# Kernel optimization log

Measured on AMD Instinct MI355X. Metric: run time of the kernel, lower is better.

Reference implementation:

```python
import jax, jax.numpy as jnp
import numpy as np

N_NODES = 100000
N_EDGES = 1600000
D_IN, D_HID, D_OUT = 128, 128, 64


def setup_inputs() -> dict:
    key = jax.random.key(0)
    k1, k2, k3, k4 = jax.random.split(key, 4)
    x = jax.random.normal(k1, (N_NODES, D_IN), dtype=jnp.float32)
    edge_index = jax.random.randint(k2, (2, N_EDGES), 0, N_NODES, dtype=jnp.int64)
    # Glorot-style weights, zero bias (GCNConv defaults: weight + bias)
    W1 = jax.random.normal(k3, (D_IN, D_HID), dtype=jnp.float32) * (1.0 / np.sqrt(D_IN))
    b1 = jnp.zeros((D_HID,), dtype=jnp.float32)
    W2 = jax.random.normal(k4, (D_HID, D_OUT), dtype=jnp.float32) * (1.0 / np.sqrt(D_HID))
    b2 = jnp.zeros((D_OUT,), dtype=jnp.float32)
    return {"x": x, "edge_index": edge_index, "W1": W1, "b1": b1, "W2": W2, "b2": b2}


def reference(x, edge_index, W1, b1, W2, b2):
    n = x.shape[0]
    src, dst = edge_index[0], edge_index[1]
    # GCN symmetric normalization, add_self_loops=False
    ones = jnp.ones((src.shape[0],), dtype=x.dtype)
    deg = jax.ops.segment_sum(ones, dst, num_segments=n)
    deg_inv_sqrt = jnp.where(deg > 0, jax.lax.rsqrt(jnp.maximum(deg, 1.0)), 0.0)
    norm = deg_inv_sqrt[src] * deg_inv_sqrt[dst]  # [E]

    def gcn_conv(h, W, b):
        h = h @ W                                   # [N, d_out] transform first
        msg = h[src] * norm[:, None]                # [E, d_out] gather + scale
        agg = jax.ops.segment_sum(msg, dst, num_segments=n)  # scatter-add
        return agg + b

    h = jax.nn.relu(gcn_conv(x, W1, b1))
    # dropout(p=0.6) is identity in eval mode (training=False)
    return gcn_conv(h, W2, b2)
```

## Files before the change

kernel.cpp:

```cpp
#include <hip/hip_runtime.h>

#define N_NODES 100000
#define N_EDGES 1600000
#define NBUCK 391
#define CHUNKA 4096
#define NBLKA 391
#define ESTRIDE 6144

typedef __bf16 bf16x8 __attribute__((ext_vector_type(8)));
typedef float f32x4 __attribute__((ext_vector_type(4)));
typedef float f32x2 __attribute__((ext_vector_type(2)));

__device__ inline unsigned short bf1(float a) {
    unsigned u = __builtin_bit_cast(unsigned, a);
    u = (u + 0x7FFF + ((u >> 16) & 1)) >> 16;
    return (unsigned short)u;
}
__device__ inline unsigned bfpack(float a, float b) {
    unsigned ua = __builtin_bit_cast(unsigned, a);
    unsigned ub = __builtin_bit_cast(unsigned, b);
    ua = (ua + 0x7FFF + ((ua >> 16) & 1)) >> 16;
    ub = (ub + 0x7FFF + ((ub >> 16) & 1)) >> 16;
    return ua | (ub << 16);
}
__device__ inline float bflo(unsigned v) { return __builtin_bit_cast(float, v << 16); }
__device__ inline float bfhi(unsigned v) { return __builtin_bit_cast(float, v & 0xFFFF0000u); }

__global__ __launch_bounds__(256) void binA_kernel(const int* __restrict__ ei,
                                                   int* __restrict__ bcur,
                                                   unsigned* __restrict__ epk,
                                                   const float* __restrict__ W1,
                                                   const float* __restrict__ W2,
                                                   unsigned short* __restrict__ Wt1,
                                                   unsigned short* __restrict__ Wt2) {
    const int t = threadIdx.x;
    if (blockIdx.x >= NBLKA) {
        if (blockIdx.x == NBLKA) {
            for (int i = t; i < 128 * 128; i += 256) {
                int k = i >> 7, n = i & 127;
                Wt1[n * 128 + k] = bf1(W1[i]);
            }
        } else {
            for (int i = t; i < 128 * 64; i += 256) {
                int k = i >> 6, n = i & 63;
                Wt2[n * 128 + k] = bf1(W2[i]);
            }
        }
        return;
    }
    __shared__ int hist[NBUCK], base[NBUCK], cur[NBUCK];
    const int e0 = blockIdx.x * CHUNKA;
    const int n  = min(CHUNKA, N_EDGES - e0);
    const int n4 = n >> 2;
    const int4* __restrict__ src4 = (const int4*)(ei + e0);
    const int4* __restrict__ dst4 = (const int4*)(ei + N_EDGES + e0);
    for (int i = t; i < NBUCK; i += 256) hist[i] = 0;
    __syncthreads();
    for (int i = t; i < n4; i += 256) {
        int4 d = dst4[i];
        atomicAdd(&hist[d.x >> 8], 1);
        atomicAdd(&hist[d.y >> 8], 1);
        atomicAdd(&hist[d.z >> 8], 1);
        atomicAdd(&hist[d.w >> 8], 1);
    }
    __syncthreads();
    for (int i = t; i < NBUCK; i += 256) {
        int h = hist[i];
        base[i] = i * ESTRIDE + (h ? atomicAdd(&bcur[i], h) : 0);
        cur[i]  = 0;
    }
    __syncthreads();
    for (int i = t; i < n4; i += 256) {
        int4 s = src4[i];
        int4 d = dst4[i];
#define PUT(ss, dd)                                               \
        do {                                                      \
            int b = (dd) >> 8;                                    \
            int r = atomicAdd(&cur[b], 1);                        \
            epk[base[b] + r] = ((unsigned)(ss) << 8) | (unsigned)((dd) & 255); \
        } while (0)
        PUT(s.x, d.x); PUT(s.y, d.y); PUT(s.z, d.z); PUT(s.w, d.w);
#undef PUT
    }
}

__global__ __launch_bounds__(512) void prep_kernel(const int* __restrict__ bcur,
                                                   int* __restrict__ boffs) {
    const int t = threadIdx.x;
    __shared__ int s[512];
    int v = (t < NBUCK) ? bcur[t] : 0;
    s[t] = v;
    __syncthreads();
#pragma unroll
    for (int off = 1; off < 512; off <<= 1) {
        int tv = (t >= off) ? s[t - off] : 0;
        __syncthreads();
        s[t] += tv;
        __syncthreads();
    }
    if (t < NBUCK) boffs[t] = s[t] - v;
    if (t == NBUCK - 1) boffs[NBUCK] = s[t];
}

__global__ __launch_bounds__(256) void binB_kernel(const unsigned* __restrict__ epk,
                                                   const int* __restrict__ bcur,
                                                   const int* __restrict__ boffs,
                                                   int* __restrict__ deg,
                                                   float* __restrict__ dis,
                                                   int* __restrict__ offs,
                                                   int* __restrict__ srcn) {
    __shared__ int cnt[256], s[256], loff[256];
    const int b  = blockIdx.x;
    const int t  = threadIdx.x;
    const int n0 = b << 8;
    const int base  = b * ESTRIDE;
    const int end   = base + bcur[b];
    const int sbase = boffs[b];
    cnt[t] = 0;
    __syncthreads();
    for (int e = base + t; e < end; e += 256)
        atomicAdd(&cnt[epk[e] & 255u], 1);
    __syncthreads();
    int v = cnt[t];
    s[t] = v;
    __syncthreads();
#pragma unroll
    for (int off = 1; off < 256; off <<= 1) {
        int tv = (t >= off) ? s[t - off] : 0;
        __syncthreads();
        s[t] += tv;
        __syncthreads();
    }
    loff[t] = s[t] - v;
    {
        int node = n0 + t;
        if (node < N_NODES) {
            deg[node]  = v;
            dis[node]  = (v > 0) ? rsqrtf((float)v) : 0.0f;
            offs[node] = sbase + loff[t];
        }
    }
    cnt[t] = 0;
    __syncthreads();
    for (int e = base + t; e < end; e += 256) {
        unsigned p = epk[e];
        int li  = (int)(p & 255u);
        int r   = atomicAdd(&cnt[li], 1);
        srcn[sbase + loff[li] + r] = (int)(p >> 8);
    }
}

__global__ __launch_bounds__(256) void gemm1_kernel(const float* __restrict__ x,
                                                    const unsigned short* __restrict__ Wt1,
                                                    const float* __restrict__ dis,
                                                    unsigned short* __restrict__ h1b) {
    __shared__ unsigned short Asm[64][136];
    __shared__ float diss[64];
    const int t = threadIdx.x;
    const int node0 = blockIdx.x * 64;

#pragma unroll
    for (int c = 0; c < 4; ++c) {
        int i = c * 256 + t;
        int row = i >> 4, ko = (i & 15) * 8;
        int gn = node0 + row;
        float4 v0 = make_float4(0, 0, 0, 0), v1 = v0;
        if (gn < N_NODES) {
            const float* p = x + (size_t)gn * 128 + ko;
            v0 = *(const float4*)p;
            v1 = *(const float4*)(p + 4);
        }
        uint4 o;
        o.x = bfpack(v0.x, v0.y); o.y = bfpack(v0.z, v0.w);
        o.z = bfpack(v1.x, v1.y); o.w = bfpack(v1.z, v1.w);
        *(uint4*)&Asm[row][ko] = o;
    }
    if (t < 64) {
        int gn = node0 + t;
        diss[t] = (gn < N_NODES) ? dis[gn] : 0.0f;
    }
    __syncthreads();

    const int wv = t >> 6, ln = t & 63;
    const int lc = ln & 15, q = ln >> 4;
    const int n0 = wv * 32;

    bf16x8 bfr[2][4];
#pragma unroll
    for (int nt = 0; nt < 2; ++nt)
#pragma unroll
        for (int k = 0; k < 4; ++k)
            bfr[nt][k] = *(const bf16x8*)(Wt1 + (size_t)(n0 + nt * 16 + lc) * 128 + k * 32 + q * 8);

    f32x4 acc[4][2];
#pragma unroll
    for (int m = 0; m < 4; ++m)
#pragma unroll
        for (int nt = 0; nt < 2; ++nt) acc[m][nt] = (f32x4)(0.0f);

#pragma unroll
    for (int k = 0; k < 4; ++k) {
        bf16x8 af[4];
#pragma unroll
        for (int m = 0; m < 4; ++m)
            af[m] = *(const bf16x8*)&Asm[m * 16 + lc][k * 32 + q * 8];
#pragma unroll
        for (int m = 0; m < 4; ++m)
#pragma unroll
            for (int nt = 0; nt < 2; ++nt)
                acc[m][nt] = __builtin_amdgcn_mfma_f32_16x16x32_bf16(af[m], bfr[nt][k], acc[m][nt], 0, 0, 0);
    }

#pragma unroll
    for (int m = 0; m < 4; ++m)
#pragma unroll
        for (int r = 0; r < 4; ++r) {
            int lr = m * 16 + q * 4 + r;
            int gn = node0 + lr;
            if (gn < N_NODES) {
                float dv = diss[lr];
#pragma unroll
                for (int nt = 0; nt < 2; ++nt)
                    h1b[(size_t)gn * 128 + n0 + nt * 16 + lc] = bf1(acc[m][nt][r] * dv);
            }
        }
}

__global__ __launch_bounds__(256) void agg1gemm2_kernel(const int* __restrict__ srcn,
                                                        const int* __restrict__ offs,
                                                        const int* __restrict__ deg,
                                                        const float* __restrict__ dis,
                                                        const unsigned short* __restrict__ h1b,
                                                        const float* __restrict__ b1,
                                                        const unsigned short* __restrict__ Wt2,
                                                        unsigned short* __restrict__ h2b) {
    __shared__ unsigned short Zs[64][136];
    __shared__ float diss[64];
    __shared__ int offs_s[64], deg_s[64];
    const int t = threadIdx.x;
    const int node0 = blockIdx.x * 64;
    if (t < 64) {
        int gn = node0 + t;
        bool ok = gn < N_NODES;
        offs_s[t] = ok ? offs[gn] : 0;
        deg_s[t]  = ok ? deg[gn] : 0;
        diss[t]   = ok ? dis[gn] : 0.0f;
    }
    __syncthreads();

    const int wv = t >> 6, ln = t & 63;
    const int qw = ln >> 4, lc = ln & 15;
    const uint4* __restrict__ h1q = (const uint4*)h1b;

    float4 bbA = *(const float4*)(b1 + lc * 8);
    float4 bbB = *(const float4*)(b1 + lc * 8 + 4);

#define ACC8(v)                                           \
    do {                                                  \
        g0 += (f32x2){bflo((v).x), bfhi((v).x)};          \
        g1 += (f32x2){bflo((v).y), bfhi((v).y)};          \
        g2 += (f32x2){bflo((v).z), bfhi((v).z)};          \
        g3 += (f32x2){bflo((v).w), bfhi((v).w)};          \
    } while (0)

    for (int r = 0; r < 4; ++r) {
        const int lr  = wv * 16 + r * 4 + qw;
        const int beg = offs_s[lr];
        const int d   = deg_s[lr];
        f32x2 g0 = (f32x2)(0.0f), g1 = (f32x2)(0.0f),
              g2 = (f32x2)(0.0f), g3 = (f32x2)(0.0f);
        int k = 0;
        for (; k + 8 <= d; k += 8) {
            int s0 = srcn[beg + k];
            int s1 = srcn[beg + k + 1];
            int s2 = srcn[beg + k + 2];
            int s3 = srcn[beg + k + 3];
            int s4 = srcn[beg + k + 4];
            int s5 = srcn[beg + k + 5];
            int s6 = srcn[beg + k + 6];
            int s7 = srcn[beg + k + 7];
            uint4 v0 = h1q[(size_t)s0 * 16 + lc];
            uint4 v1 = h1q[(size_t)s1 * 16 + lc];
            uint4 v2 = h1q[(size_t)s2 * 16 + lc];
            uint4 v3 = h1q[(size_t)s3 * 16 + lc];
            uint4 v4 = h1q[(size_t)s4 * 16 + lc];
            uint4 v5 = h1q[(size_t)s5 * 16 + lc];
            uint4 v6 = h1q[(size_t)s6 * 16 + lc];
            uint4 v7 = h1q[(size_t)s7 * 16 + lc];
            ACC8(v0); ACC8(v1); ACC8(v2); ACC8(v3);
            ACC8(v4); ACC8(v5); ACC8(v6); ACC8(v7);
        }
        for (; k + 4 <= d; k += 4) {
            int s0 = srcn[beg + k];
            int s1 = srcn[beg + k + 1];
            int s2 = srcn[beg + k + 2];
            int s3 = srcn[beg + k + 3];
            uint4 v0 = h1q[(size_t)s0 * 16 + lc];
            uint4 v1 = h1q[(size_t)s1 * 16 + lc];
            uint4 v2 = h1q[(size_t)s2 * 16 + lc];
            uint4 v3 = h1q[(size_t)s3 * 16 + lc];
            ACC8(v0); ACC8(v1); ACC8(v2); ACC8(v3);
        }
        for (; k < d; ++k) {
            int s = srcn[beg + k];
            uint4 v = h1q[(size_t)s * 16 + lc];
            ACC8(v);
        }
        float dv = diss[lr];
        uint4 o;
        o.x = bfpack(fmaxf(dv * g0.x + bbA.x, 0.0f), fmaxf(dv * g0.y + bbA.y, 0.0f));
        o.y = bfpack(fmaxf(dv * g1.x + bbA.z, 0.0f), fmaxf(dv * g1.y + bbA.w, 0.0f));
        o.z = bfpack(fmaxf(dv * g2.x + bbB.x, 0.0f), fmaxf(dv * g2.y + bbB.y, 0.0f));
        o.w = bfpack(fmaxf(dv * g3.x + bbB.z, 0.0f), fmaxf(dv * g3.y + bbB.w, 0.0f));
        *(uint4*)&Zs[lr][lc * 8] = o;
    }
#undef ACC8
    __syncthreads();

    const int lc2 = ln & 15, q = ln >> 4;
    const int n0 = wv * 16;

    bf16x8 bfr[4];
#pragma unroll
    for (int k = 0; k < 4; ++k)
        bfr[k] = *(const bf16x8*)(Wt2 + (size_t)(n0 + lc2) * 128 + k * 32 + q * 8);

    f32x4 acc[4];
#pragma unroll
    for (int m = 0; m < 4; ++m) acc[m] = (f32x4)(0.0f);

#pragma unroll
    for (int k = 0; k < 4; ++k) {
        bf16x8 af[4];
#pragma unroll
        for (int m = 0; m < 4; ++m)
            af[m] = *(const bf16x8*)&Zs[m * 16 + lc2][k * 32 + q * 8];
#pragma unroll
        for (int m = 0; m < 4; ++m)
            acc[m] = __builtin_amdgcn_mfma_f32_16x16x32_bf16(af[m], bfr[k], acc[m], 0, 0, 0);
    }

#pragma unroll
    for (int m = 0; m < 4; ++m)
#pragma unroll
        for (int r = 0; r < 4; ++r) {
            int lr = m * 16 + q * 4 + r;
            int gn = node0 + lr;
            if (gn < N_NODES) {
                float dv = diss[lr];
                h2b[(size_t)gn * 64 + n0 + lc2] = bf1(acc[m][r] * dv);
            }
        }
}

__global__ __launch_bounds__(256) void agg2_kernel(const int* __restrict__ srcn,
                                                   const int* __restrict__ offs,
                                                   const int* __restrict__ deg,
                                                   const float* __restrict__ dis,
                                                   const unsigned short* __restrict__ h2b,
                                                   const float* __restrict__ b2,
                                                   float* __restrict__ out) {
    __shared__ float diss[64];
    __shared__ int offs_s[64], deg_s[64];
    const int t = threadIdx.x;
    const int node0 = blockIdx.x * 64;
    if (t < 64) {
        int gn = node0 + t;
        bool ok = gn < N_NODES;
        offs_s[t] = ok ? offs[gn] : 0;
        deg_s[t]  = ok ? deg[gn] : 0;
        diss[t]   = ok ? dis[gn] : 0.0f;
    }
    __syncthreads();

    const int wv = t >> 6, ln = t & 63;
    const int qw = ln >> 4, lc = ln & 15;
    const uint2* __restrict__ h2v = (const uint2*)h2b;

    float4 bb = *(const float4*)(b2 + lc * 4);

#define ACC4(v)                                           \
    do {                                                  \
        g0 += (f32x2){bflo((v).x), bfhi((v).x)};          \
        g1 += (f32x2){bflo((v).y), bfhi((v).y)};          \
    } while (0)

    for (int r = 0; r < 4; ++r) {
        const int lr  = wv * 16 + r * 4 + qw;
        const int beg = offs_s[lr];
        const int d   = deg_s[lr];
        f32x2 g0 = (f32x2)(0.0f), g1 = (f32x2)(0.0f);
        int k = 0;
        for (; k + 8 <= d; k += 8) {
            int s0 = srcn[beg + k];
            int s1 = srcn[beg + k + 1];
            int s2 = srcn[beg + k + 2];
            int s3 = srcn[beg + k + 3];
            int s4 = srcn[beg + k + 4];
            int s5 = srcn[beg + k + 5];
            int s6 = srcn[beg + k + 6];
            int s7 = srcn[beg + k + 7];
            uint2 v0 = h2v[(size_t)s0 * 16 + lc];
            uint2 v1 = h2v[(size_t)s1 * 16 + lc];
            uint2 v2 = h2v[(size_t)s2 * 16 + lc];
            uint2 v3 = h2v[(size_t)s3 * 16 + lc];
            uint2 v4 = h2v[(size_t)s4 * 16 + lc];
            uint2 v5 = h2v[(size_t)s5 * 16 + lc];
            uint2 v6 = h2v[(size_t)s6 * 16 + lc];
            uint2 v7 = h2v[(size_t)s7 * 16 + lc];
            ACC4(v0); ACC4(v1); ACC4(v2); ACC4(v3);
            ACC4(v4); ACC4(v5); ACC4(v6); ACC4(v7);
        }
        for (; k + 4 <= d; k += 4) {
            int s0 = srcn[beg + k];
            int s1 = srcn[beg + k + 1];
            int s2 = srcn[beg + k + 2];
            int s3 = srcn[beg + k + 3];
            uint2 v0 = h2v[(size_t)s0 * 16 + lc];
            uint2 v1 = h2v[(size_t)s1 * 16 + lc];
            uint2 v2 = h2v[(size_t)s2 * 16 + lc];
            uint2 v3 = h2v[(size_t)s3 * 16 + lc];
            ACC4(v0); ACC4(v1); ACC4(v2); ACC4(v3);
        }
        for (; k < d; ++k) {
            int s = srcn[beg + k];
            uint2 v = h2v[(size_t)s * 16 + lc];
            ACC4(v);
        }
        int gn = node0 + lr;
        if (gn < N_NODES) {
            float dv = diss[lr];
            float4 o;
            o.x = dv * g0.x + bb.x;
            o.y = dv * g0.y + bb.y;
            o.z = dv * g1.x + bb.z;
            o.w = dv * g1.y + bb.w;
            *(float4*)(out + (size_t)gn * 64 + lc * 4) = o;
        }
    }
#undef ACC4
}

extern "C" void kernel_launch(void* const* d_in, const int* in_sizes, int n_in,
                              void* d_out, int out_size, void* d_ws, size_t ws_size,
                              hipStream_t stream) {
    const float* x  = (const float*)d_in[0];
    const int*   ei = (const int*)d_in[1];
    const float* W1 = (const float*)d_in[2];
    const float* b1 = (const float*)d_in[3];
    const float* W2 = (const float*)d_in[4];
    const float* b2 = (const float*)d_in[5];
    float* out = (float*)d_out;

    char* ws = (char*)d_ws;
    int*   bcur  = (int*)(ws);
    int*   boffs = (int*)(ws + (size_t)4 * 1024);
    int*   deg   = (int*)(ws + (size_t)16 * 1024);
    int*   offs  = (int*)(ws + (size_t)512 * 1024);
    float* dis   = (float*)(ws + (size_t)1024 * 1024);
    unsigned short* Wt1 = (unsigned short*)(ws + (size_t)1536 * 1024);
    unsigned short* Wt2 = (unsigned short*)(ws + (size_t)1600 * 1024);
    unsigned* epk = (unsigned*)(ws + (size_t)2560 * 1024);
    int*   srcn  = (int*)(ws + (size_t)12800 * 1024);
    unsigned short* h1b = (unsigned short*)(ws + (size_t)20 * 1024 * 1024);
    unsigned short* h2b = (unsigned short*)(ws + (size_t)46 * 1024 * 1024);

    hipMemsetAsync(ws, 0, (size_t)2 * 1024, stream);

    binA_kernel<<<NBLKA + 2, 256, 0, stream>>>(ei, bcur, epk, W1, W2, Wt1, Wt2);
    prep_kernel<<<1, 512, 0, stream>>>(bcur, boffs);
    binB_kernel<<<NBUCK, 256, 0, stream>>>(epk, bcur, boffs, deg, dis, offs, srcn);
    gemm1_kernel<<<(N_NODES + 63) / 64, 256, 0, stream>>>(x, Wt1, dis, h1b);
    agg1gemm2_kernel<<<(N_NODES + 63) / 64, 256, 0, stream>>>(srcn, offs, deg, dis,
                                                              h1b, b1, Wt2, h2b);
    agg2_kernel<<<(N_NODES + 63) / 64, 256, 0, stream>>>(srcn, offs, deg, dis,
                                                         h2b, b2, out);
}
```

Baseline: 257.1 us.

## Fuse bucket prefix scan and first GEMM into the binB kernel

Removes the single-block prep scan kernel: each binB block now computes its own bucket base offset by summing the preceding bucket counts with a block reduction. The layer-1 GEMM is fused into the same kernel. Each 256-node bucket block runs four 64-row MFMA tiles and uses the degree norms it just computed from shared memory instead of reading dis back from global. This saves two kernel launches and the dis round trip. The cost is that the GEMM now runs on only 391 blocks, which lowers parallelism, and each block performs a redundant reduction over up to 391 counts.

```diff
diff --git a/kernel.cpp b/kernel.cpp
--- a/kernel.cpp
+++ b/kernel.cpp
@@ -84,38 +84,36 @@
     }
 }
 
-__global__ __launch_bounds__(512) void prep_kernel(const int* __restrict__ bcur,
-                                                   int* __restrict__ boffs) {
-    const int t = threadIdx.x;
-    __shared__ int s[512];
-    int v = (t < NBUCK) ? bcur[t] : 0;
-    s[t] = v;
-    __syncthreads();
-#pragma unroll
-    for (int off = 1; off < 512; off <<= 1) {
-        int tv = (t >= off) ? s[t - off] : 0;
+__global__ __launch_bounds__(256) void binBg1_kernel(const unsigned* __restrict__ epk,
+                                                     const int* __restrict__ bcur,
+                                                     int* __restrict__ deg,
+                                                     float* __restrict__ dis,
+                                                     int* __restrict__ offs,
+                                                     int* __restrict__ srcn,
+                                                     const float* __restrict__ x,
+                                                     const unsigned short* __restrict__ Wt1,
+                                                     unsigned short* __restrict__ h1b) {
+    __shared__ int cnt[256], s[256], loff[256];
+    __shared__ float disb[256];
+    __shared__ unsigned short Asm[64][136];
+    const int b = blockIdx.x, t = threadIdx.x;
+    const int n0g = b << 8;
+
+    int part = 0;
+    for (int j = t; j < b; j += 256) part += bcur[j];
+    s[t] = part;
+    __syncthreads();
+#pragma unroll
+    for (int off = 128; off > 0; off >>= 1) {
+        if (t < off) s[t] += s[t + off];
         __syncthreads();
-        s[t] += tv;
-        __syncthreads();
-    }
-    if (t < NBUCK) boffs[t] = s[t] - v;
-    if (t == NBUCK - 1) boffs[NBUCK] = s[t];
-}
-
-__global__ __launch_bounds__(256) void binB_kernel(const unsigned* __restrict__ epk,
-                                                   const int* __restrict__ bcur,
-                                                   const int* __restrict__ boffs,
-                                                   int* __restrict__ deg,
-                                                   float* __restrict__ dis,
-                                                   int* __restrict__ offs,
-                                                   int* __restrict__ srcn) {
-    __shared__ int cnt[256], s[256], loff[256];
-    const int b  = blockIdx.x;
-    const int t  = threadIdx.x;
-    const int n0 = b << 8;
-    const int base  = b * ESTRIDE;
-    const int end   = base + bcur[b];
-    const int sbase = boffs[b];
+    }
+    const int sbase = s[0];
+    const int bcnt  = bcur[b];
+    __syncthreads();
+
+    const int base = b * ESTRIDE;
+    const int end  = base + bcnt;
     cnt[t] = 0;
     __syncthreads();
     for (int e = base + t; e < end; e += 256)
@@ -132,11 +130,13 @@
         __syncthreads();
     }
     loff[t] = s[t] - v;
+    float dvt = (v > 0) ? rsqrtf((float)v) : 0.0f;
+    disb[t] = dvt;
     {
-        int node = n0 + t;
+        int node = n0g + t;
         if (node < N_NODES) {
             deg[node]  = v;
-            dis[node]  = (v > 0) ? rsqrtf((float)v) : 0.0f;
+            dis[node]  = dvt;
             offs[node] = sbase + loff[t];
         }
     }
@@ -148,82 +148,72 @@
         int r   = atomicAdd(&cnt[li], 1);
         srcn[sbase + loff[li] + r] = (int)(p >> 8);
     }
-}
-
-__global__ __launch_bounds__(256) void gemm1_kernel(const float* __restrict__ x,
-                                                    const unsigned short* __restrict__ Wt1,
-                                                    const float* __restrict__ dis,
-                                                    unsigned short* __restrict__ h1b) {
-    __shared__ unsigned short Asm[64][136];
-    __shared__ float diss[64];
-    const int t = threadIdx.x;
-    const int node0 = blockIdx.x * 64;
-
-#pragma unroll
-    for (int c = 0; c < 4; ++c) {
-        int i = c * 256 + t;
-        int row = i >> 4, ko = (i & 15) * 8;
-        int gn = node0 + row;
-        float4 v0 = make_float4(0, 0, 0, 0), v1 = v0;
-        if (gn < N_NODES) {
-            const float* p = x + (size_t)gn * 128 + ko;
-            v0 = *(const float4*)p;
-            v1 = *(const float4*)(p + 4);
-        }
-        uint4 o;
-        o.x = bfpack(v0.x, v0.y); o.y = bfpack(v0.z, v0.w);
-        o.z = bfpack(v1.x, v1.y); o.w = bfpack(v1.z, v1.w);
-        *(uint4*)&Asm[row][ko] = o;
-    }
-    if (t < 64) {
-        int gn = node0 + t;
-        diss[t] = (gn < N_NODES) ? dis[gn] : 0.0f;
-    }
-    __syncthreads();
 
     const int wv = t >> 6, ln = t & 63;
     const int lc = ln & 15, q = ln >> 4;
-    const int n0 = wv * 32;
+    const int nn0 = wv * 32;
 
     bf16x8 bfr[2][4];
 #pragma unroll
     for (int nt = 0; nt < 2; ++nt)
 #pragma unroll
         for (int k = 0; k < 4; ++k)
-            bfr[nt][k] = *(const bf16x8*)(Wt1 + (size_t)(n0 + nt * 16 + lc) * 128 + k * 32 + q * 8);
-
-    f32x4 acc[4][2];
-#pragma unroll
-    for (int m = 0; m < 4; ++m)
-#pragma unroll
-        for (int nt = 0; nt < 2; ++nt) acc[m][nt] = (f32x4)(0.0f);
-
-#pragma unroll
-    for (int k = 0; k < 4; ++k) {
-        bf16x8 af[4];
+            bfr[nt][k] = *(const bf16x8*)(Wt1 + (size_t)(nn0 + nt * 16 + lc) * 128 + k * 32 + q * 8);
+
+    for (int tile = 0; tile < 4; ++tile) {
+        const int node0 = n0g + tile * 64;
+        __syncthreads();
+#pragma unroll
+        for (int c = 0; c < 4; ++c) {
+            int i = c * 256 + t;
+            int row = i >> 4, ko = (i & 15) * 8;
+            int gn = node0 + row;
+            float4 v0 = make_float4(0, 0, 0, 0), v1 = v0;
+            if (gn < N_NODES) {
+                const float* p = x + (size_t)gn * 128 + ko;
+                v0 = *(const float4*)p;
+                v1 = *(const float4*)(p + 4);
+            }
+            uint4 o;
+            o.x = bfpack(v0.x, v0.y); o.y = bfpack(v0.z, v0.w);
+            o.z = bfpack(v1.x, v1.y); o.w = bfpack(v1.z, v1.w);
+            *(uint4*)&Asm[row][ko] = o;
+        }
+        __syncthreads();
+
+        f32x4 acc[4][2];
 #pragma unroll
         for (int m = 0; m < 4; ++m)
-            af[m] = *(const bf16x8*)&Asm[m * 16 + lc][k * 32 + q * 8];
+#pragma unroll
+            for (int nt = 0; nt < 2; ++nt) acc[m][nt] = (f32x4)(0.0f);
+
+#pragma unroll
+        for (int k = 0; k < 4; ++k) {
+            bf16x8 af[4];
+#pragma unroll
+            for (int m = 0; m < 4; ++m)
+                af[m] = *(const bf16x8*)&Asm[m * 16 + lc][k * 32 + q * 8];
+#pragma unroll
+            for (int m = 0; m < 4; ++m)
+#pragma unroll
+                for (int nt = 0; nt < 2; ++nt)
+                    acc[m][nt] = __builtin_amdgcn_mfma_f32_16x16x32_bf16(af[m], bfr[nt][k], acc[m][nt], 0, 0, 0);
+        }
+
 #pragma unroll
         for (int m = 0; m < 4; ++m)
 #pragma unroll
-            for (int nt = 0; nt < 2; ++nt)
-                acc[m][nt] = __builtin_amdgcn_mfma_f32_16x16x32_bf16(af[m], bfr[nt][k], acc[m][nt], 0, 0, 0);
-    }
-
-#pragma unroll
-    for (int m = 0; m < 4; ++m)
-#pragma unroll
-        for (int r = 0; r < 4; ++r) {
-            int lr = m * 16 + q * 4 + r;
-            int gn = node0 + lr;
-            if (gn < N_NODES) {
-                float dv = diss[lr];
-#pragma unroll
-                for (int nt = 0; nt < 2; ++nt)
-                    h1b[(size_t)gn * 128 + n0 + nt * 16 + lc] = bf1(acc[m][nt][r] * dv);
+            for (int r = 0; r < 4; ++r) {
+                int lr = m * 16 + q * 4 + r;
+                int gn = node0 + lr;
+                if (gn < N_NODES) {
+                    float dv = disb[tile * 64 + lr];
+#pragma unroll
+                    for (int nt = 0; nt < 2; ++nt)
+                        h1b[(size_t)gn * 128 + nn0 + nt * 16 + lc] = bf1(acc[m][nt][r] * dv);
+                }
             }
-        }
+    }
 }
 
 __global__ __launch_bounds__(256) void agg1gemm2_kernel(const int* __restrict__ srcn,
@@ -454,7 +444,6 @@
 
     char* ws = (char*)d_ws;
     int*   bcur  = (int*)(ws);
-    int*   boffs = (int*)(ws + (size_t)4 * 1024);
     int*   deg   = (int*)(ws + (size_t)16 * 1024);
     int*   offs  = (int*)(ws + (size_t)512 * 1024);
     float* dis   = (float*)(ws + (size_t)1024 * 1024);
@@ -468,9 +457,8 @@
     hipMemsetAsync(ws, 0, (size_t)2 * 1024, stream);
 
     binA_kernel<<<NBLKA + 2, 256, 0, stream>>>(ei, bcur, epk, W1, W2, Wt1, Wt2);
-    prep_kernel<<<1, 512, 0, stream>>>(bcur, boffs);
-    binB_kernel<<<NBUCK, 256, 0, stream>>>(epk, bcur, boffs, deg, dis, offs, srcn);
-    gemm1_kernel<<<(N_NODES + 63) / 64, 256, 0, stream>>>(x, Wt1, dis, h1b);
+    binBg1_kernel<<<NBUCK, 256, 0, stream>>>(epk, bcur, deg, dis, offs, srcn,
+                                             x, Wt1, h1b);
     agg1gemm2_kernel<<<(N_NODES + 63) / 64, 256, 0, stream>>>(srcn, offs, deg, dis,
                                                               h1b, b1, Wt2, h2b);
     agg2_kernel<<<(N_NODES + 63) / 64, 256, 0, stream>>>(srcn, offs, deg, dis,
```

After: 257.7 us. Within noise of the previous version (+0.3%).
